# Optimization experiments

Measured on AMD Instinct MI355X. Metric: run time of the kernel, lower is better.

Reference implementation:

```python
import jax, jax.numpy as jnp
import numpy as np

D_MODEL = 1024
N_HEADS = 16
D_K = D_MODEL // N_HEADS
LN_EPS = 1e-5
NEG_INF = -1.0e9


def setup_inputs() -> dict:
    key = jax.random.key(0)
    ks = jax.random.split(key, 10)
    B, S, D = 8, 1024, D_MODEL
    scale = 1.0 / np.sqrt(D)
    return {
        "input_Q": jax.random.normal(ks[0], (B, S, D), jnp.float32),
        "input_K": jax.random.normal(ks[1], (B, S, D), jnp.float32),
        "input_V": jax.random.normal(ks[2], (B, S, D), jnp.float32),
        "attn_mask": jax.random.bernoulli(ks[3], 0.1, (B, S, S)),  # True = masked
        # torch Linear weights: [out_features, in_features]
        "W_Q": jax.random.normal(ks[4], (D, D), jnp.float32) * scale,
        "W_K": jax.random.normal(ks[5], (D, D), jnp.float32) * scale,
        "W_V": jax.random.normal(ks[6], (D, D), jnp.float32) * scale,
        "W_fc": jax.random.normal(ks[7], (D, D), jnp.float32) * scale,
        "ln_gamma": jnp.ones((D,), jnp.float32),
        "ln_beta": jnp.zeros((D,), jnp.float32),
    }


def _layer_norm(x, gamma, beta):
    mu = jnp.mean(x, axis=-1, keepdims=True)
    var = jnp.mean(jnp.square(x - mu), axis=-1, keepdims=True)
    return (x - mu) * jax.lax.rsqrt(var + LN_EPS) * gamma + beta


def reference(input_Q, input_K, input_V, attn_mask, W_Q, W_K, W_V, W_fc, ln_gamma, ln_beta):
    B, S, D = input_Q.shape
    # project and split heads: [B, H, S, d_k]
    def proj(x, W):
        return jnp.einsum('bsd,od->bso', x, W).reshape(B, -1, N_HEADS, D_K).transpose(0, 2, 1, 3)
    Q = proj(input_Q, W_Q)
    K = proj(input_K, W_K)
    V = proj(input_V, W_V)
    scores = jnp.einsum('bhqk,bhmk->bhqm', Q, K) / np.sqrt(D_K)  # [B,H,Sq,Sk]
    scores = jnp.where(attn_mask[:, None, :, :], NEG_INF, scores)
    attn = jax.nn.softmax(scores, axis=-1)
    context = jnp.einsum('bhqm,bhmd->bhqd', attn, V)
    context = context.transpose(0, 2, 1, 3).reshape(B, -1, N_HEADS * D_K)
    output = jnp.einsum('bsd,od->bso', context, W_fc)
    out = _layer_norm(output + input_Q, ln_gamma, ln_beta)
    return out, attn
```

## Files before the change

### kernel.cpp

```cpp
#include <hip/hip_runtime.h>

typedef __attribute__((ext_vector_type(8))) __bf16 bf16x8;
typedef __attribute__((ext_vector_type(4))) float f32x4;

#define SLEN 1024
#define DMODEL 1024
#define NHEADS 16
#define DKH 64
#define BATCH 8

__device__ __forceinline__ unsigned short f2bf(float f) {
  unsigned u = __builtin_bit_cast(unsigned, f);
  u += 0x7FFFu + ((u >> 16) & 1u);
  return (unsigned short)(u >> 16);
}

__device__ __forceinline__ void gload_lds16(const void* g, void* l) {
  __builtin_amdgcn_global_load_lds((const __attribute__((address_space(1))) unsigned int*)g,
                                   (__attribute__((address_space(3))) unsigned int*)l, 16, 0, 0);
}

__global__ void detect_mask(const unsigned char* __restrict__ m, int* __restrict__ flag) {
  int t = threadIdx.x;
  unsigned any = 0;
  for (int j = t; j < 4096; j += 64) any |= m[j * 4 + 1];
  unsigned long long b = __ballot(any != 0);
  if (t == 0) *flag = (b != 0) ? 1 : 0;
}

__global__ __launch_bounds__(256) void mask_pack(const unsigned char* __restrict__ m,
                                                 const int* __restrict__ flagp,
                                                 unsigned* __restrict__ mb) {
  long base = (long)blockIdx.x << 10;
  int tid = threadIdx.x;
  int flag = *flagp;
  unsigned nib;
  if (flag) {
    uchar4 v = ((const uchar4*)(m + base))[tid];
    nib = (v.x ? 1u : 0u) | (v.y ? 2u : 0u) | (v.z ? 4u : 0u) | (v.w ? 8u : 0u);
  } else {
    int4 v = ((const int4*)((const int*)m + base))[tid];
    nib = (v.x ? 1u : 0u) | (v.y ? 2u : 0u) | (v.z ? 4u : 0u) | (v.w ? 8u : 0u);
  }
  __shared__ unsigned char nibs[256];
  nibs[tid] = (unsigned char)nib;
  __syncthreads();
  if (tid < 32) {
    unsigned wv = 0;
#pragma unroll
    for (int i = 0; i < 8; i++) wv |= ((unsigned)nibs[tid * 8 + i]) << (i * 4);
    mb[((long)blockIdx.x << 5) + tid] = wv;
  }
}

__global__ __launch_bounds__(256) void cvt_all(
    const float* __restrict__ i0, const float* __restrict__ i1,
    const float* __restrict__ i2, const float* __restrict__ w0,
    const float* __restrict__ w1, const float* __restrict__ w2,
    const float* __restrict__ w3, unsigned short* __restrict__ xo0,
    unsigned short* __restrict__ xo1, unsigned short* __restrict__ xo2,
    unsigned short* __restrict__ wo0, unsigned short* __restrict__ wo1,
    unsigned short* __restrict__ wo2, unsigned short* __restrict__ wo3,
    int n8x, int n8w) {
  int which = blockIdx.y;
  const float* in;
  unsigned short* o;
  int n8;
  if (which < 3) {
    in = which == 0 ? i0 : which == 1 ? i1 : i2;
    o = which == 0 ? xo0 : which == 1 ? xo1 : xo2;
    n8 = n8x;
  } else {
    in = which == 3 ? w0 : which == 4 ? w1 : which == 5 ? w2 : w3;
    o = which == 3 ? wo0 : which == 4 ? wo1 : which == 5 ? wo2 : wo3;
    n8 = n8w;
  }
  int i = blockIdx.x * 256 + threadIdx.x;
  if (i >= n8) return;
  const float4* p = (const float4*)in;
  float4 f0 = p[2 * i], f1 = p[2 * i + 1];
  union { unsigned short us[8]; uint4 v; } pk;
  pk.us[0] = f2bf(f0.x); pk.us[1] = f2bf(f0.y); pk.us[2] = f2bf(f0.z); pk.us[3] = f2bf(f0.w);
  pk.us[4] = f2bf(f1.x); pk.us[5] = f2bf(f1.y); pk.us[6] = f2bf(f1.z); pk.us[7] = f2bf(f1.w);
  ((uint4*)o)[i] = pk.v;
}

__global__ __launch_bounds__(256) void gemm_proj3(
    const unsigned short* __restrict__ A0, const unsigned short* __restrict__ A1,
    const unsigned short* __restrict__ A2, const unsigned short* __restrict__ B0,
    const unsigned short* __restrict__ B1, const unsigned short* __restrict__ B2,
    unsigned short* __restrict__ O0, unsigned short* __restrict__ O1,
    unsigned short* __restrict__ O2) {
  const int z = blockIdx.z;
  const unsigned short* Ab = z == 0 ? A0 : z == 1 ? A1 : A2;
  const unsigned short* Bb = z == 0 ? B0 : z == 1 ? B1 : B2;
  unsigned short* obf = z == 0 ? O0 : z == 1 ? O1 : O2;
  const float scale = z == 0 ? 0.125f : 1.0f;

  const int m0 = blockIdx.x * 128;
  const int n0 = blockIdx.y * 128;
  const int tid = threadIdx.x;
  const int l = tid & 63;
  const int w = tid >> 6;
  const int wr = w >> 1, wc = w & 1;
  const int rl = l & 15, hi = l >> 4;

  __shared__ __attribute__((aligned(16))) unsigned short As[128 * 64];
  __shared__ __attribute__((aligned(16))) unsigned short Bs[128 * 64];

  f32x4 acc[4][4];
#pragma unroll
  for (int i = 0; i < 4; i++)
#pragma unroll
    for (int j = 0; j < 4; j++) acc[i][j] = f32x4{0.f, 0.f, 0.f, 0.f};

  for (int k0 = 0; k0 < 1024; k0 += 64) {
    __syncthreads();
#pragma unroll
    for (int i = 0; i < 4; i++) {
      int o = (i * 256 + tid) * 16;
      int row = o >> 7, cb = o & 127;
      int cbs = cb ^ ((row & 7) << 4);
      gload_lds16(Ab + (long)(m0 + row) * 1024 + k0 + (cbs >> 1), (char*)As + o);
    }
#pragma unroll
    for (int i = 0; i < 4; i++) {
      int o = (i * 256 + tid) * 16;
      int row = o >> 7, cb = o & 127;
      int cbs = cb ^ ((row & 7) << 4);
      gload_lds16(Bb + (long)(n0 + row) * 1024 + k0 + (cbs >> 1), (char*)Bs + o);
    }
    __syncthreads();

#pragma unroll
    for (int ks = 0; ks < 2; ks++) {
      int kb = ks * 64 + hi * 16;
      bf16x8 af[4], bfr[4];
#pragma unroll
      for (int mi = 0; mi < 4; mi++) {
        int row = wr * 64 + mi * 16 + rl;
        af[mi] = *(const bf16x8*)((const char*)As + row * 128 + (kb ^ ((row & 7) << 4)));
      }
#pragma unroll
      for (int ni = 0; ni < 4; ni++) {
        int row = wc * 64 + ni * 16 + rl;
        bfr[ni] = *(const bf16x8*)((const char*)Bs + row * 128 + (kb ^ ((row & 7) << 4)));
      }
#pragma unroll
      for (int mi = 0; mi < 4; mi++)
#pragma unroll
        for (int ni = 0; ni < 4; ni++)
          acc[mi][ni] = __builtin_amdgcn_mfma_f32_16x16x32_bf16(af[mi], bfr[ni], acc[mi][ni], 0, 0, 0);
    }
  }

  const int r0 = hi << 2;
#pragma unroll
  for (int mi = 0; mi < 4; mi++) {
#pragma unroll
    for (int ni = 0; ni < 4; ni++) {
      f32x4 v = acc[mi][ni];
      int row = m0 + wr * 64 + mi * 16 + r0;
      int col = n0 + wc * 64 + ni * 16 + rl;
      if (z == 2) {
        union { unsigned short us[4]; unsigned long long vv; } pk;
        pk.us[0] = f2bf(v[0]); pk.us[1] = f2bf(v[1]);
        pk.us[2] = f2bf(v[2]); pk.us[3] = f2bf(v[3]);
        long idx = ((long)(((row >> 10) * 16 + (col >> 6)) * 64 + (col & 63)) << 10) + (row & 1023);
        *(unsigned long long*)&obf[idx] = pk.vv;
      } else {
#pragma unroll
        for (int j = 0; j < 4; j++) {
          int rr = row + j;
          long idx = (((long)((rr >> 10) * 16 + (col >> 6)) * 1024 + (rr & 1023)) << 6) + (col & 63);
          obf[idx] = f2bf(v[j] * scale);
        }
      }
    }
  }
}

__global__ __launch_bounds__(256) void gemm_fc(
    const unsigned short* __restrict__ Ab, const unsigned short* __restrict__ Bb,
    float* __restrict__ of32) {
  const int m0 = blockIdx.x * 128;
  const int n0 = blockIdx.y * 128;
  const int tid = threadIdx.x;
  const int l = tid & 63;
  const int w = tid >> 6;
  const int wr = w >> 1, wc = w & 1;
  const int rl = l & 15, hi = l >> 4;

  __shared__ __attribute__((aligned(16))) unsigned short As[128 * 64];
  __shared__ __attribute__((aligned(16))) unsigned short Bs[128 * 64];

  f32x4 acc[4][4];
#pragma unroll
  for (int i = 0; i < 4; i++)
#pragma unroll
    for (int j = 0; j < 4; j++) acc[i][j] = f32x4{0.f, 0.f, 0.f, 0.f};

  for (int k0 = 0; k0 < 1024; k0 += 64) {
    __syncthreads();
#pragma unroll
    for (int i = 0; i < 4; i++) {
      int o = (i * 256 + tid) * 16;
      int row = o >> 7, cb = o & 127;
      int cbs = cb ^ ((row & 7) << 4);
      gload_lds16(Ab + (long)(m0 + row) * 1024 + k0 + (cbs >> 1), (char*)As + o);
    }
#pragma unroll
    for (int i = 0; i < 4; i++) {
      int o = (i * 256 + tid) * 16;
      int row = o >> 7, cb = o & 127;
      int cbs = cb ^ ((row & 7) << 4);
      gload_lds16(Bb + (long)(n0 + row) * 1024 + k0 + (cbs >> 1), (char*)Bs + o);
    }
    __syncthreads();

#pragma unroll
    for (int ks = 0; ks < 2; ks++) {
      int kb = ks * 64 + hi * 16;
      bf16x8 af[4], bfr[4];
#pragma unroll
      for (int mi = 0; mi < 4; mi++) {
        int row = wr * 64 + mi * 16 + rl;
        af[mi] = *(const bf16x8*)((const char*)As + row * 128 + (kb ^ ((row & 7) << 4)));
      }
#pragma unroll
      for (int ni = 0; ni < 4; ni++) {
        int row = wc * 64 + ni * 16 + rl;
        bfr[ni] = *(const bf16x8*)((const char*)Bs + row * 128 + (kb ^ ((row & 7) << 4)));
      }
#pragma unroll
      for (int mi = 0; mi < 4; mi++)
#pragma unroll
        for (int ni = 0; ni < 4; ni++)
          acc[mi][ni] = __builtin_amdgcn_mfma_f32_16x16x32_bf16(af[mi], bfr[ni], acc[mi][ni], 0, 0, 0);
    }
  }

  const int r0 = hi << 2;
#pragma unroll
  for (int mi = 0; mi < 4; mi++) {
#pragma unroll
    for (int ni = 0; ni < 4; ni++) {
      f32x4 v = acc[mi][ni];
      int row = m0 + wr * 64 + mi * 16 + r0;
      int col = n0 + wc * 64 + ni * 16 + rl;
#pragma unroll
      for (int j = 0; j < 4; j++)
        of32[((long)(row + j) << 10) + col] = v[j];
    }
  }
}

__global__ __launch_bounds__(512) void attn_fused2(
    const unsigned short* __restrict__ Qh, const unsigned short* __restrict__ Kh,
    const unsigned short* __restrict__ Vt, const unsigned* __restrict__ mb,
    float* __restrict__ attn, unsigned short* __restrict__ ctx) {
  const int lin = blockIdx.x;
  const int xcd = lin & 7;
  const int k_ = lin >> 3;
  const int z = xcd + ((k_ >> 3) << 3);
  const int qt = k_ & 7;
  const int b = z >> 4, h = z & 15;
  const int tid = threadIdx.x, l = tid & 63, w = tid >> 6;
  const int rl = l & 15, hi = l >> 4;

  __shared__ __attribute__((aligned(16))) unsigned short Pl[16 * 1024];
  __shared__ float redm[8][16], reds[8][16];
  __shared__ __attribute__((aligned(16))) float Pp[4][64][4];

  const long bh = (long)z * (SLEN * DKH);
  const unsigned short* Kb = Kh + bh;
  const unsigned short* Vb = Vt + bh;
  const long abase = (long)z << 20;

  bf16x8 qf0, qf1;
  {
    const unsigned short* qp = Qh + bh + (long)(qt * 128 + rl) * 64 + hi * 8;
    qf0 = *(const bf16x8*)qp;
    qf1 = *(const bf16x8*)(qp + 32);
  }

  for (int s = 0; s < 8; s++) {
    const int q0 = qt * 128 + s * 16;

    f32x4 acc[8];
#pragma unroll
    for (int t = 0; t < 8; t++) acc[t] = f32x4{0.f, 0.f, 0.f, 0.f};

    __builtin_amdgcn_s_setprio(1);
#pragma unroll
    for (int t = 0; t < 8; t++) {
      int col = w * 128 + t * 16 + rl;
      const unsigned short* kp = Kb + (long)col * 64 + hi * 8;
      bf16x8 k0 = *(const bf16x8*)kp;
      bf16x8 k1 = *(const bf16x8*)(kp + 32);
      acc[t] = __builtin_amdgcn_mfma_f32_16x16x32_bf16(k0, qf0, acc[t], 0, 0, 0);
      acc[t] = __builtin_amdgcn_mfma_f32_16x16x32_bf16(k1, qf1, acc[t], 0, 0, 0);
    }
    __builtin_amdgcn_s_setprio(0);

    unsigned mw[4];
    {
      uint4 w0 = *(const uint4*)(mb + (((long)((b << 10) | (q0 + rl))) << 5) + w * 4);
      mw[0] = w0.x; mw[1] = w0.y; mw[2] = w0.z; mw[3] = w0.w;
    }

    float mx = -3.0e38f;
#pragma unroll
    for (int t = 0; t < 8; t++) {
#pragma unroll
      for (int j = 0; j < 4; j++) {
        unsigned bit = (mw[t >> 1] >> (((t & 1) << 4) + (hi << 2) + j)) & 1u;
        float v = bit ? -1.0e9f : acc[t][j];
        acc[t][j] = v;
        mx = fmaxf(mx, v);
      }
    }
    mx = fmaxf(mx, __shfl_xor(mx, 16));
    mx = fmaxf(mx, __shfl_xor(mx, 32));
    float sum = 0.f;
#pragma unroll
    for (int t = 0; t < 8; t++)
#pragma unroll
      for (int j = 0; j < 4; j++) {
        float e = __expf(acc[t][j] - mx);
        acc[t][j] = e;
        sum += e;
      }
    sum += __shfl_xor(sum, 16);
    sum += __shfl_xor(sum, 32);
    if (hi == 0) { redm[w][rl] = mx; reds[w][rl] = sum; }
    __syncthreads();
    float M, S, inv;
    {
      M = -3.0e38f;
#pragma unroll
      for (int ww = 0; ww < 8; ww++) M = fmaxf(M, redm[ww][rl]);
      S = 0.f;
#pragma unroll
      for (int ww = 0; ww < 8; ww++) S += reds[ww][rl] * __expf(redm[ww][rl] - M);
      inv = __expf(mx - M) / S;
    }

#pragma unroll
    for (int t = 0; t < 8; t++) {
      int c0 = w * 128 + t * 16 + hi * 4;
      union { unsigned short us[4]; unsigned long long v; } pk;
      pk.us[0] = f2bf(acc[t][0] * inv);
      pk.us[1] = f2bf(acc[t][1] * inv);
      pk.us[2] = f2bf(acc[t][2] * inv);
      pk.us[3] = f2bf(acc[t][3] * inv);
      *(unsigned long long*)((char*)Pl + rl * 2048 + ((c0 * 2) ^ ((rl & 7) << 4))) = pk.v;
    }
    __syncthreads();

    {
      const int half = tid >> 8;
      const int t8 = tid & 255;
      const long arow = abase + ((long)q0 << 10) + t8 * 4;
#pragma unroll
      for (int i = 0; i < 8; i++) {
        int row = i * 2 + half;
        unsigned long long pv8 = *(const unsigned long long*)(
            (const char*)Pl + row * 2048 + ((t8 * 8) ^ ((row & 7) << 4)));
        f32x4 o4;
        o4[0] = __builtin_bit_cast(float, (unsigned)((pv8 & 0xFFFFu) << 16));
        o4[1] = __builtin_bit_cast(float, (unsigned)(((pv8 >> 16) & 0xFFFFu) << 16));
        o4[2] = __builtin_bit_cast(float, (unsigned)(((pv8 >> 32) & 0xFFFFu) << 16));
        o4[3] = __builtin_bit_cast(float, (unsigned)(((pv8 >> 48) & 0xFFFFu) << 16));
        __builtin_nontemporal_store(o4, (f32x4*)&attn[arow + ((long)row << 10)]);
      }
    }

    if (s < 7) {
      const unsigned short* qp = Qh + bh + (long)(q0 + 16 + rl) * 64 + hi * 8;
      qf0 = *(const bf16x8*)qp;
      qf1 = *(const bf16x8*)(qp + 32);
    }

    const int d4 = w & 3, kh = w >> 2;
    f32x4 c2 = f32x4{0.f, 0.f, 0.f, 0.f};
    __builtin_amdgcn_s_setprio(1);
#pragma unroll
    for (int k16 = 0; k16 < 16; k16++) {
      int ks = kh * 16 + k16;
      bf16x8 af = *(const bf16x8*)((const char*)Pl + rl * 2048 + ((ks * 64 + hi * 16) ^ ((rl & 7) << 4)));
      bf16x8 vf = *(const bf16x8*)(Vb + (long)(d4 * 16 + rl) * 1024 + ks * 32 + hi * 8);
      c2 = __builtin_amdgcn_mfma_f32_16x16x32_bf16(af, vf, c2, 0, 0, 0);
    }
    __builtin_amdgcn_s_setprio(0);

    if (w < 4) {
      *(f32x4*)Pp[w][l] = c2;
    }
    __syncthreads();
    if (w >= 4) {
      f32x4 p = *(const f32x4*)Pp[w - 4][l];
#pragma unroll
      for (int j = 0; j < 4; j++) {
        __builtin_nontemporal_store(
            f2bf(c2[j] + p[j]),
            &ctx[((long)(b * 1024 + q0 + hi * 4 + j) << 10) + h * 64 + d4 * 16 + rl]);
      }
    }
  }
}

__global__ __launch_bounds__(256) void ln_kernel(const float* __restrict__ fc,
                                                 const float* __restrict__ inQ,
                                                 const float* __restrict__ gamma,
                                                 const float* __restrict__ beta,
                                                 float* __restrict__ out) {
  long base = (long)blockIdx.x << 10;
  int tid = threadIdx.x, l = tid & 63, w = tid >> 6;
  float4 a = ((const float4*)(fc + base))[tid];
  float4 b = ((const float4*)(inQ + base))[tid];
  float4 x; x.x = a.x + b.x; x.y = a.y + b.y; x.z = a.z + b.z; x.w = a.w + b.w;
  float s = x.x + x.y + x.z + x.w;
  float q = x.x * x.x + x.y * x.y + x.z * x.z + x.w * x.w;
  for (int o = 32; o; o >>= 1) { s += __shfl_xor(s, o); q += __shfl_xor(q, o); }
  __shared__ float rs[4], rq[4];
  if (l == 0) { rs[w] = s; rq[w] = q; }
  __syncthreads();
  s = rs[0] + rs[1] + rs[2] + rs[3];
  q = rq[0] + rq[1] + rq[2] + rq[3];
  float mu = s * (1.0f / 1024.0f);
  float var = q * (1.0f / 1024.0f) - mu * mu;
  float rstd = rsqrtf(var + 1e-5f);
  float4 g = ((const float4*)gamma)[tid];
  float4 be = ((const float4*)beta)[tid];
  float4 o4;
  o4.x = (x.x - mu) * rstd * g.x + be.x;
  o4.y = (x.y - mu) * rstd * g.y + be.y;
  o4.z = (x.z - mu) * rstd * g.z + be.z;
  o4.w = (x.w - mu) * rstd * g.w + be.w;
  ((float4*)(out + base))[tid] = o4;
}

extern "C" void kernel_launch(void* const* d_in, const int* in_sizes, int n_in,
                              void* d_out, int out_size, void* d_ws, size_t ws_size,
                              hipStream_t stream) {
  const float* inQ = (const float*)d_in[0];
  const float* inK = (const float*)d_in[1];
  const float* inV = (const float*)d_in[2];
  const unsigned char* mask = (const unsigned char*)d_in[3];
  const float* WQ = (const float*)d_in[4];
  const float* WK = (const float*)d_in[5];
  const float* WV = (const float*)d_in[6];
  const float* WFC = (const float*)d_in[7];
  const float* gamma = (const float*)d_in[8];
  const float* beta = (const float*)d_in[9];

  float* out = (float*)d_out;
  float* attn = out + (size_t)BATCH * SLEN * DMODEL;

  char* ws = (char*)d_ws;
  size_t off = 256;
  int* flag = (int*)ws;
  auto take = [&](size_t bytes) { char* p = ws + off; off += (bytes + 255) & ~255UL; return p; };
  const size_t XB = (size_t)BATCH * SLEN * DMODEL * 2;
  const size_t WB = (size_t)DMODEL * DMODEL * 2;
  unsigned short* Xq = (unsigned short*)take(XB);
  unsigned short* Xk = (unsigned short*)take(XB);
  unsigned short* Xv = (unsigned short*)take(XB);
  unsigned short* Wqb = (unsigned short*)take(WB);
  unsigned short* Wkb = (unsigned short*)take(WB);
  unsigned short* Wvb = (unsigned short*)take(WB);
  unsigned short* Wfcb = (unsigned short*)take(WB);
  unsigned short* Qh = (unsigned short*)take(XB);
  unsigned short* Kh = (unsigned short*)take(XB);
  unsigned short* Vt = (unsigned short*)take(XB);
  unsigned short* ctx = (unsigned short*)take(XB);
  float* fc = (float*)take((size_t)BATCH * SLEN * DMODEL * 4);
  unsigned* mb = (unsigned*)take((size_t)BATCH * SLEN * 32 * 4);

  detect_mask<<<1, 64, 0, stream>>>(mask, flag);
  mask_pack<<<BATCH * SLEN, 256, 0, stream>>>(mask, flag, mb);

  const int n8x = BATCH * SLEN * DMODEL / 8;
  const int n8w = DMODEL * DMODEL / 8;
  cvt_all<<<dim3(n8x / 256, 7), 256, 0, stream>>>(inQ, inK, inV, WQ, WK, WV, WFC,
                                                  Xq, Xk, Xv, Wqb, Wkb, Wvb, Wfcb,
                                                  n8x, n8w);

  gemm_proj3<<<dim3(64, 8, 3), 256, 0, stream>>>(Xq, Xk, Xv, Wqb, Wkb, Wvb, Qh, Kh, Vt);

  attn_fused2<<<dim3(1024), 512, 0, stream>>>(Qh, Kh, Vt, mb, attn, ctx);

  gemm_fc<<<dim3(64, 8), 256, 0, stream>>>(ctx, Wfcb, fc);

  ln_kernel<<<BATCH * SLEN, 256, 0, stream>>>(fc, inQ, gamma, beta, out);
}
```

Before: 306.1 us.

## Fuse output projection GEMM with residual add and LayerNorm

Replaces the separate fc GEMM and LayerNorm kernels with one kernel where each 512-thread block computes 32 full rows of the output projection. The residual add, row mean and variance reduction, and normalization then run in registers and shared memory. This removes the fp32 fc intermediate write and read and one kernel launch. In exchange, weight fragments are read directly from global memory with no LDS staging or reuse across blocks, only 256 blocks are launched, and the tile shape is much narrower in M.

Measured after the change: 349.9 us. 1.14x slower.

```diff
diff --git a/kernel.cpp b/kernel.cpp
--- a/kernel.cpp
+++ b/kernel.cpp
@@ -180,77 +180,118 @@
   }
 }
 
-__global__ __launch_bounds__(256) void gemm_fc(
-    const unsigned short* __restrict__ Ab, const unsigned short* __restrict__ Bb,
-    float* __restrict__ of32) {
-  const int m0 = blockIdx.x * 128;
-  const int n0 = blockIdx.y * 128;
+__global__ __launch_bounds__(512) void gemm_fc_ln(
+    const unsigned short* __restrict__ ctx, const unsigned short* __restrict__ Wfc,
+    const float* __restrict__ inQ, const float* __restrict__ gamma,
+    const float* __restrict__ beta, float* __restrict__ out) {
+  const int m0 = blockIdx.x * 32;
   const int tid = threadIdx.x;
-  const int l = tid & 63;
-  const int w = tid >> 6;
-  const int wr = w >> 1, wc = w & 1;
+  const int l = tid & 63, w = tid >> 6;
   const int rl = l & 15, hi = l >> 4;
 
-  __shared__ __attribute__((aligned(16))) unsigned short As[128 * 64];
-  __shared__ __attribute__((aligned(16))) unsigned short Bs[128 * 64];
-
-  f32x4 acc[4][4];
-#pragma unroll
-  for (int i = 0; i < 4; i++)
-#pragma unroll
-    for (int j = 0; j < 4; j++) acc[i][j] = f32x4{0.f, 0.f, 0.f, 0.f};
+  __shared__ __attribute__((aligned(16))) unsigned short As[32 * 64];
+  __shared__ float rsum[8][32], rsq[8][32];
+
+  f32x4 acc[2][8];
+#pragma unroll
+  for (int i = 0; i < 2; i++)
+#pragma unroll
+    for (int j = 0; j < 8; j++) acc[i][j] = f32x4{0.f, 0.f, 0.f, 0.f};
 
   for (int k0 = 0; k0 < 1024; k0 += 64) {
     __syncthreads();
-#pragma unroll
-    for (int i = 0; i < 4; i++) {
-      int o = (i * 256 + tid) * 16;
+    if (tid < 256) {
+      int o = tid * 16;
       int row = o >> 7, cb = o & 127;
       int cbs = cb ^ ((row & 7) << 4);
-      gload_lds16(Ab + (long)(m0 + row) * 1024 + k0 + (cbs >> 1), (char*)As + o);
-    }
-#pragma unroll
-    for (int i = 0; i < 4; i++) {
-      int o = (i * 256 + tid) * 16;
-      int row = o >> 7, cb = o & 127;
-      int cbs = cb ^ ((row & 7) << 4);
-      gload_lds16(Bb + (long)(n0 + row) * 1024 + k0 + (cbs >> 1), (char*)Bs + o);
+      gload_lds16(ctx + (long)(m0 + row) * 1024 + k0 + (cbs >> 1), (char*)As + o);
     }
     __syncthreads();
 
 #pragma unroll
     for (int ks = 0; ks < 2; ks++) {
       int kb = ks * 64 + hi * 16;
-      bf16x8 af[4], bfr[4];
-#pragma unroll
-      for (int mi = 0; mi < 4; mi++) {
-        int row = wr * 64 + mi * 16 + rl;
+      bf16x8 af[2];
+#pragma unroll
+      for (int mi = 0; mi < 2; mi++) {
+        int row = mi * 16 + rl;
         af[mi] = *(const bf16x8*)((const char*)As + row * 128 + (kb ^ ((row & 7) << 4)));
       }
 #pragma unroll
-      for (int ni = 0; ni < 4; ni++) {
-        int row = wc * 64 + ni * 16 + rl;
-        bfr[ni] = *(const bf16x8*)((const char*)Bs + row * 128 + (kb ^ ((row & 7) << 4)));
-      }
-#pragma unroll
-      for (int mi = 0; mi < 4; mi++)
-#pragma unroll
-        for (int ni = 0; ni < 4; ni++)
-          acc[mi][ni] = __builtin_amdgcn_mfma_f32_16x16x32_bf16(af[mi], bfr[ni], acc[mi][ni], 0, 0, 0);
-    }
-  }
-
-  const int r0 = hi << 2;
-#pragma unroll
-  for (int mi = 0; mi < 4; mi++) {
-#pragma unroll
-    for (int ni = 0; ni < 4; ni++) {
-      f32x4 v = acc[mi][ni];
-      int row = m0 + wr * 64 + mi * 16 + r0;
-      int col = n0 + wc * 64 + ni * 16 + rl;
-#pragma unroll
-      for (int j = 0; j < 4; j++)
-        of32[((long)(row + j) << 10) + col] = v[j];
+      for (int ni = 0; ni < 8; ni++) {
+        int bn = w * 128 + ni * 16 + rl;
+        bf16x8 bf = *(const bf16x8*)(Wfc + (long)bn * 1024 + k0 + ks * 32 + hi * 8);
+#pragma unroll
+        for (int mi = 0; mi < 2; mi++)
+          acc[mi][ni] = __builtin_amdgcn_mfma_f32_16x16x32_bf16(af[mi], bf, acc[mi][ni], 0, 0, 0);
+      }
+    }
+  }
+
+  float s[2][4], q2[2][4];
+#pragma unroll
+  for (int mi = 0; mi < 2; mi++)
+#pragma unroll
+    for (int j = 0; j < 4; j++) { s[mi][j] = 0.f; q2[mi][j] = 0.f; }
+#pragma unroll
+  for (int mi = 0; mi < 2; mi++) {
+#pragma unroll
+    for (int ni = 0; ni < 8; ni++) {
+      int col = w * 128 + ni * 16 + rl;
+#pragma unroll
+      for (int j = 0; j < 4; j++) {
+        int r = mi * 16 + hi * 4 + j;
+        float x = acc[mi][ni][j] + inQ[(long)(m0 + r) * 1024 + col];
+        acc[mi][ni][j] = x;
+        s[mi][j] += x;
+        q2[mi][j] += x * x;
+      }
+    }
+  }
+#pragma unroll
+  for (int mi = 0; mi < 2; mi++)
+#pragma unroll
+    for (int j = 0; j < 4; j++) {
+      s[mi][j] += __shfl_xor(s[mi][j], 1);  q2[mi][j] += __shfl_xor(q2[mi][j], 1);
+      s[mi][j] += __shfl_xor(s[mi][j], 2);  q2[mi][j] += __shfl_xor(q2[mi][j], 2);
+      s[mi][j] += __shfl_xor(s[mi][j], 4);  q2[mi][j] += __shfl_xor(q2[mi][j], 4);
+      s[mi][j] += __shfl_xor(s[mi][j], 8);  q2[mi][j] += __shfl_xor(q2[mi][j], 8);
+    }
+  if (rl == 0) {
+#pragma unroll
+    for (int mi = 0; mi < 2; mi++)
+#pragma unroll
+      for (int j = 0; j < 4; j++) {
+        int r = mi * 16 + hi * 4 + j;
+        rsum[w][r] = s[mi][j];
+        rsq[w][r] = q2[mi][j];
+      }
+  }
+  __syncthreads();
+  float mu[2][4], rstd[2][4];
+#pragma unroll
+  for (int mi = 0; mi < 2; mi++)
+#pragma unroll
+    for (int j = 0; j < 4; j++) {
+      int r = mi * 16 + hi * 4 + j;
+      float ss = 0.f, qq = 0.f;
+#pragma unroll
+      for (int ww = 0; ww < 8; ww++) { ss += rsum[ww][r]; qq += rsq[ww][r]; }
+      mu[mi][j] = ss * (1.0f / 1024.0f);
+      float var = qq * (1.0f / 1024.0f) - mu[mi][j] * mu[mi][j];
+      rstd[mi][j] = rsqrtf(var + 1e-5f);
+    }
+#pragma unroll
+  for (int mi = 0; mi < 2; mi++) {
+#pragma unroll
+    for (int ni = 0; ni < 8; ni++) {
+      int col = w * 128 + ni * 16 + rl;
+      float g = gamma[col], be = beta[col];
+#pragma unroll
+      for (int j = 0; j < 4; j++) {
+        int r = mi * 16 + hi * 4 + j;
+        out[(long)(m0 + r) * 1024 + col] = (acc[mi][ni][j] - mu[mi][j]) * rstd[mi][j] * g + be;
+      }
     }
   }
 }
@@ -408,37 +449,6 @@
       }
     }
   }
-}
-
-__global__ __launch_bounds__(256) void ln_kernel(const float* __restrict__ fc,
-                                                 const float* __restrict__ inQ,
-                                                 const float* __restrict__ gamma,
-                                                 const float* __restrict__ beta,
-                                                 float* __restrict__ out) {
-  long base = (long)blockIdx.x << 10;
-  int tid = threadIdx.x, l = tid & 63, w = tid >> 6;
-  float4 a = ((const float4*)(fc + base))[tid];
-  float4 b = ((const float4*)(inQ + base))[tid];
-  float4 x; x.x = a.x + b.x; x.y = a.y + b.y; x.z = a.z + b.z; x.w = a.w + b.w;
-  float s = x.x + x.y + x.z + x.w;
-  float q = x.x * x.x + x.y * x.y + x.z * x.z + x.w * x.w;
-  for (int o = 32; o; o >>= 1) { s += __shfl_xor(s, o); q += __shfl_xor(q, o); }
-  __shared__ float rs[4], rq[4];
-  if (l == 0) { rs[w] = s; rq[w] = q; }
-  __syncthreads();
-  s = rs[0] + rs[1] + rs[2] + rs[3];
-  q = rq[0] + rq[1] + rq[2] + rq[3];
-  float mu = s * (1.0f / 1024.0f);
-  float var = q * (1.0f / 1024.0f) - mu * mu;
-  float rstd = rsqrtf(var + 1e-5f);
-  float4 g = ((const float4*)gamma)[tid];
-  float4 be = ((const float4*)beta)[tid];
-  float4 o4;
-  o4.x = (x.x - mu) * rstd * g.x + be.x;
-  o4.y = (x.y - mu) * rstd * g.y + be.y;
-  o4.z = (x.z - mu) * rstd * g.z + be.z;
-  o4.w = (x.w - mu) * rstd * g.w + be.w;
-  ((float4*)(out + base))[tid] = o4;
 }
 
 extern "C" void kernel_launch(void* const* d_in, const int* in_sizes, int n_in,
@@ -475,7 +485,6 @@
   unsigned short* Kh = (unsigned short*)take(XB);
   unsigned short* Vt = (unsigned short*)take(XB);
   unsigned short* ctx = (unsigned short*)take(XB);
-  float* fc = (float*)take((size_t)BATCH * SLEN * DMODEL * 4);
   unsigned* mb = (unsigned*)take((size_t)BATCH * SLEN * 32 * 4);
 
   detect_mask<<<1, 64, 0, stream>>>(mask, flag);
@@ -491,7 +500,5 @@
 
   attn_fused2<<<dim3(1024), 512, 0, stream>>>(Qh, Kh, Vt, mb, attn, ctx);
 
-  gemm_fc<<<dim3(64, 8), 256, 0, stream>>>(ctx, Wfcb, fc);
-
-  ln_kernel<<<BATCH * SLEN, 256, 0, stream>>>(fc, inQ, gamma, beta, out);
-}
+  gemm_fc_ln<<<dim3(256), 512, 0, stream>>>(ctx, Wfcb, inQ, gamma, beta, out);
+}
```
